# Kernel optimization log

Hardware: AMD Instinct MI355X
Metric: run time of the kernel (lower is better)

The kernel has to match this reference:

```python
import jax, jax.numpy as jnp
import numpy as np

NEG_SLOPE = 0.2


def setup_inputs() -> dict:
    key = jax.random.key(0)
    ks = jax.random.split(key, 10)
    V, E, Din, Dout, H = 50000, 800000, 128, 128, 4
    h = jax.random.normal(ks[0], (V, Din), dtype=jnp.float32)
    edge_index = jax.random.randint(ks[1], (2, E), 0, V, dtype=jnp.int32)
    edge_weight = jax.random.uniform(ks[2], (E,), dtype=jnp.float32)
    s = 1.0 / np.sqrt(Din)
    Wq = jax.random.normal(ks[3], (Din, Dout), dtype=jnp.float32) * s
    Wk = jax.random.normal(ks[4], (Din, Dout), dtype=jnp.float32) * s
    Wv = jax.random.normal(ks[5], (Din, Dout), dtype=jnp.float32) * s
    Wo = jax.random.normal(ks[6], (Dout, Dout), dtype=jnp.float32) * (1.0 / np.sqrt(Dout))
    We = jax.random.normal(ks[7], (1, H), dtype=jnp.float32)
    bq = jnp.zeros((Dout,), jnp.float32)
    bk = jnp.zeros((Dout,), jnp.float32)
    bv = jnp.zeros((Dout,), jnp.float32)
    bo = jnp.zeros((Dout,), jnp.float32)
    be = jnp.zeros((H,), jnp.float32)
    return {"h": h, "edge_index": edge_index, "edge_weight": edge_weight,
            "Wq": Wq, "bq": bq, "Wk": Wk, "bk": bk, "Wv": Wv, "bv": bv,
            "Wo": Wo, "bo": bo, "We": We, "be": be}


def reference(h, edge_index, edge_weight, Wq, bq, Wk, bk, Wv, bv, Wo, bo, We, be):
    V = h.shape[0]
    H = be.shape[0]
    Dout = Wq.shape[1]
    F_h = Dout // H

    # Node projections -> [V, H, F_h]
    Q = (h @ Wq + bq).reshape(V, H, F_h)
    K = (h @ Wk + bk).reshape(V, H, F_h)
    Vv = (h @ Wv + bv).reshape(V, H, F_h)

    # Edge bias: Linear(1, H) on edge_weight, then LeakyReLU -> [E, H]
    edge_bias = jax.nn.leaky_relu(edge_weight[:, None] @ We + be, negative_slope=NEG_SLOPE)

    src, tgt = edge_index[0], edge_index[1]

    # Per-edge attention logits: dot(Q[src], K[tgt]) / sqrt(F_h) + bias -> [E, H]
    attn_raw = jnp.sum(Q[src] * K[tgt], axis=-1) / jnp.sqrt(jnp.float32(F_h)) + edge_bias
    attn_exp = jnp.exp(attn_raw)  # faithful: original uses unshifted exp

    # Scatter-softmax normalizer per target node -> [V, H]
    deg = jax.ops.segment_sum(attn_exp, tgt, num_segments=V) + 1e-16
    attn_norm = attn_exp / deg[tgt]  # [E, H]

    # Weighted messages and scatter-sum to targets
    msg = Vv[src] * attn_norm[:, :, None] * edge_weight[:, None, None]  # [E, H, F_h]
    out = jax.ops.segment_sum(msg, tgt, num_segments=V)  # [V, H, F_h]

    out = out.reshape(V, H * F_h)
    out = jax.nn.leaky_relu(out @ Wo + bo, negative_slope=NEG_SLOPE)
    return out
```

## Files before the change

kernel.cpp:

```cpp
#include <hip/hip_runtime.h>
#include <hip/hip_bf16.h>

#define NEG_SLOPE 0.2f

typedef __attribute__((ext_vector_type(8))) short bf16x8;
typedef __attribute__((ext_vector_type(4))) float f32x4;

__device__ __forceinline__ void splitf(float x, unsigned short& h, unsigned short& l)
{
    const unsigned int u  = __float_as_uint(x);
    const unsigned int uh = (u + 0x7fffu + ((u >> 16) & 1u)) >> 16;
    const float        fh = __uint_as_float(uh << 16);
    const float        r  = x - fh;
    const unsigned int ur = __float_as_uint(r);
    const unsigned int ul = (ur + 0x7fffu + ((ur >> 16) & 1u)) >> 16;
    h = (unsigned short)uh;
    l = (unsigned short)ul;
}

__global__ __launch_bounds__(256) void wsplit(const float* __restrict__ W,
                                              unsigned short* __restrict__ Wth,
                                              unsigned short* __restrict__ Wtl)
{
    const int t = blockIdx.x * 256 + threadIdx.x;
    const int k = t >> 7, n = t & 127;
    unsigned short h, l;
    splitf(W[k * 128 + n], h, l);
    Wth[n * 128 + k] = h;
    Wtl[n * 128 + k] = l;
}

__global__ __launch_bounds__(256) void gemm_mfma(
    const float* __restrict__ A,
    const unsigned short* __restrict__ Bh0, const unsigned short* __restrict__ Bl0,
    const unsigned short* __restrict__ Bh1, const unsigned short* __restrict__ Bl1,
    const unsigned short* __restrict__ Bh2, const unsigned short* __restrict__ Bl2,
    const float* __restrict__ b0, const float* __restrict__ b1, const float* __restrict__ b2,
    float* __restrict__ D0, float* __restrict__ D1, float* __restrict__ D2,
    int V, int lrelu)
{
    __shared__ unsigned short Ash[64][40], Asl[64][40];
    __shared__ unsigned short Bsh[128][40], Bsl[128][40];

    const int m = blockIdx.y;
    const unsigned short* __restrict__ Wth = (m == 0) ? Bh0 : ((m == 1) ? Bh1 : Bh2);
    const unsigned short* __restrict__ Wtl = (m == 0) ? Bl0 : ((m == 1) ? Bl1 : Bl2);
    const float* __restrict__ bias         = (m == 0) ? b0  : ((m == 1) ? b1  : b2);
    float* __restrict__ D                  = (m == 0) ? D0  : ((m == 1) ? D1  : D2);

    const int tid  = threadIdx.x;
    const int w    = tid >> 6;
    const int l    = tid & 63;
    const int row0 = blockIdx.x * 64;

    const int srow = tid >> 2;
    const int skc  = tid & 3;

    f32x4 acc[8];
#pragma unroll
    for (int t = 0; t < 8; ++t) acc[t] = (f32x4){0.f, 0.f, 0.f, 0.f};

    for (int k0 = 0; k0 < 128; k0 += 32) {
        {
            const int gr = row0 + srow;
            float x[8] = {0.f, 0.f, 0.f, 0.f, 0.f, 0.f, 0.f, 0.f};
            if (gr < V) {
                const float4 a0 = *(const float4*)(A + (size_t)gr * 128 + k0 + skc * 8);
                const float4 a1 = *(const float4*)(A + (size_t)gr * 128 + k0 + skc * 8 + 4);
                x[0] = a0.x; x[1] = a0.y; x[2] = a0.z; x[3] = a0.w;
                x[4] = a1.x; x[5] = a1.y; x[6] = a1.z; x[7] = a1.w;
            }
            bf16x8 vh, vl;
#pragma unroll
            for (int i = 0; i < 8; ++i) {
                unsigned short hh, ll;
                splitf(x[i], hh, ll);
                vh[i] = (short)hh; vl[i] = (short)ll;
            }
            *(bf16x8*)&Ash[srow][skc * 8] = vh;
            *(bf16x8*)&Asl[srow][skc * 8] = vl;
        }
#pragma unroll
        for (int r = 0; r < 2; ++r) {
            const int idx = tid + r * 256;
            const int n = idx >> 2, bkc = idx & 3;
            *(bf16x8*)&Bsh[n][bkc * 8] = *(const bf16x8*)(Wth + n * 128 + k0 + bkc * 8);
            *(bf16x8*)&Bsl[n][bkc * 8] = *(const bf16x8*)(Wtl + n * 128 + k0 + bkc * 8);
        }
        __syncthreads();

        const int ar  = w * 16 + (l & 15);
        const int kc8 = (l >> 4) * 8;
        const bf16x8 ah = *(const bf16x8*)&Ash[ar][kc8];
        const bf16x8 al = *(const bf16x8*)&Asl[ar][kc8];
#pragma unroll
        for (int t = 0; t < 8; ++t) {
            const int col = t * 16 + (l & 15);
            const bf16x8 bh = *(const bf16x8*)&Bsh[col][kc8];
            const bf16x8 bl = *(const bf16x8*)&Bsl[col][kc8];
            acc[t] = __builtin_amdgcn_mfma_f32_16x16x32_bf16(ah, bh, acc[t], 0, 0, 0);
            acc[t] = __builtin_amdgcn_mfma_f32_16x16x32_bf16(ah, bl, acc[t], 0, 0, 0);
            acc[t] = __builtin_amdgcn_mfma_f32_16x16x32_bf16(al, bh, acc[t], 0, 0, 0);
        }
        __syncthreads();
    }

    const int colb = l & 15;
    const int rsub = (l >> 4) * 4;
#pragma unroll
    for (int t = 0; t < 8; ++t) {
        const int col = t * 16 + colb;
        const float bv = bias[col];
#pragma unroll
        for (int r = 0; r < 4; ++r) {
            const int grow = row0 + w * 16 + rsub + r;
            if (grow < V) {
                float xx = acc[t][r] + bv;
                if (lrelu) xx = (xx > 0.f) ? xx : NEG_SLOPE * xx;
                D[(size_t)grow * 128 + col] = xx;
            }
        }
    }
}

__global__ __launch_bounds__(256) void count_tgt(const int* __restrict__ tgt,
                                                 int* __restrict__ cnt, int E)
{
    const int e = blockIdx.x * blockDim.x + threadIdx.x;
    if (e < E) atomicAdd(cnt + tgt[e], 1);
}

__global__ __launch_bounds__(256) void scan1(const int* __restrict__ cnt,
                                             int* __restrict__ offs,
                                             int* __restrict__ bsums, int V)
{
    __shared__ int sh[256];
    const int t = threadIdx.x;
    const int base = blockIdx.x * 1024;
    int v[4];
    int s = 0;
#pragma unroll
    for (int i = 0; i < 4; ++i) {
        const int idx = base + t * 4 + i;
        v[i] = (idx < V) ? cnt[idx] : 0;
        s += v[i];
    }
    sh[t] = s;
    __syncthreads();
    for (int off = 1; off < 256; off <<= 1) {
        const int x = (t >= off) ? sh[t - off] : 0;
        __syncthreads();
        sh[t] += x;
        __syncthreads();
    }
    int run = (t > 0) ? sh[t - 1] : 0;
#pragma unroll
    for (int i = 0; i < 4; ++i) {
        const int idx = base + t * 4 + i;
        if (idx < V) offs[idx] = run;
        run += v[i];
    }
    if (t == 255) bsums[blockIdx.x] = sh[255];
}

__global__ void scan2(int* __restrict__ bsums, int nb)
{
    if (threadIdx.x == 0 && blockIdx.x == 0) {
        int run = 0;
        for (int i = 0; i < nb; ++i) { const int x = bsums[i]; bsums[i] = run; run += x; }
    }
}

__global__ __launch_bounds__(256) void scan3(int* __restrict__ offs,
                                             const int* __restrict__ bsums,
                                             int* __restrict__ fill, int V)
{
    const int v = blockIdx.x * blockDim.x + threadIdx.x;
    if (v >= V) return;
    const int o = offs[v] + bsums[v >> 10];
    offs[v] = o;
    fill[v] = o;
}

__global__ __launch_bounds__(256) void scatter_edges(
    const int* __restrict__ src, const int* __restrict__ tgt,
    const float* __restrict__ ew, int* __restrict__ fill,
    int2* __restrict__ se, int E)
{
    const int e = blockIdx.x * blockDim.x + threadIdx.x;
    if (e >= E) return;
    const int pos = atomicAdd(fill + tgt[e], 1);
    se[pos] = make_int2(src[e], __float_as_int(ew[e]));
}

__global__ __launch_bounds__(256) void fused_agg(
    const float* __restrict__ Q, const float* __restrict__ K,
    const float* __restrict__ Vv, const int2* __restrict__ se,
    const int* __restrict__ offs, const int* __restrict__ fill,
    const float* __restrict__ Wei, const float* __restrict__ bei,
    float* __restrict__ accum, int V)
{
    __shared__ float Ksh[4][4][36];
    const int wid = threadIdx.x >> 6;
    const int node = blockIdx.x * 4 + wid;
    if (node >= V) return;
    const int l   = threadIdx.x & 63;
    const int h   = l & 3;
    const int hd  = l >> 4;
    const float weH = Wei[h], beH = bei[h];
    const float2* __restrict__ Vv2 = (const float2*)Vv;

    {
        const float2 kk = *(const float2*)(K + (size_t)node * 128 + l * 2);
        const int f0 = l * 2;
        Ksh[wid][f0 >> 5][f0 & 31] = kk.x;
        Ksh[wid][(f0 + 1) >> 5][(f0 + 1) & 31] = kk.y;
    }

    const int start = offs[node];
    const int end   = fill[node];

    float degacc = 0.f;
    float ax = 0.f, ay = 0.f;

    for (int b0 = start; b0 < end; b0 += 16) {
        const int nj = min(16, end - b0);
        const int jj = l >> 2;
        int   s = 0;
        float w = 0.f, p = 0.f;
        if (jj < nj) {
            const int2 t = se[b0 + jj];
            s = t.x;
            w = __int_as_float(t.y);
            const float4* qp = (const float4*)(Q + (size_t)s * 128 + h * 32);
            float dot = 0.f;
#pragma unroll
            for (int i = 0; i < 8; ++i) {
                const float4 q = qp[i];
                const float4 k = *(const float4*)&Ksh[wid][h][i * 4];
                dot += q.x * k.x + q.y * k.y + q.z * k.z + q.w * k.w;
            }
            float bb = fmaf(w, weH, beH);
            bb = (bb > 0.f) ? bb : NEG_SLOPE * bb;
            p = __expf(fmaf(dot, 0.17677669529663687f, bb));
        }
        degacc += p;
        const float coef = p * w;

        if (nj == 16) {
#pragma unroll
            for (int j = 0; j < 16; ++j) {
                const float cj = __shfl(coef, j * 4 + hd);
                const int   sj = __shfl(s,    j * 4);
                const float2 v = Vv2[(size_t)sj * 64 + l];
                ax = fmaf(cj, v.x, ax);
                ay = fmaf(cj, v.y, ay);
            }
        } else {
            for (int j = 0; j < nj; ++j) {
                const float cj = __shfl(coef, j * 4 + hd);
                const int   sj = __shfl(s,    j * 4);
                const float2 v = Vv2[(size_t)sj * 64 + l];
                ax = fmaf(cj, v.x, ax);
                ay = fmaf(cj, v.y, ay);
            }
        }
    }

    float d = degacc;
    d += __shfl_xor(d, 4);
    d += __shfl_xor(d, 8);
    d += __shfl_xor(d, 16);
    d += __shfl_xor(d, 32);
    const float deg = __shfl(d, hd);
    const float inv = 1.0f / (deg + 1e-16f);

    *(float2*)(accum + (size_t)node * 128 + l * 2) =
        make_float2(ax * inv, ay * inv);
}

extern "C" void kernel_launch(void* const* d_in, const int* in_sizes, int n_in,
                              void* d_out, int out_size, void* d_ws, size_t ws_size,
                              hipStream_t stream)
{
    const float* h   = (const float*)d_in[0];
    const int*   ei  = (const int*)  d_in[1];
    const float* ew  = (const float*)d_in[2];
    const float* Wq  = (const float*)d_in[3];
    const float* bq  = (const float*)d_in[4];
    const float* Wk  = (const float*)d_in[5];
    const float* bk  = (const float*)d_in[6];
    const float* Wv  = (const float*)d_in[7];
    const float* bv  = (const float*)d_in[8];
    const float* Wo  = (const float*)d_in[9];
    const float* bo  = (const float*)d_in[10];
    const float* Wei = (const float*)d_in[11];
    const float* bei = (const float*)d_in[12];

    const int V = in_sizes[0] / 128;
    const int E = in_sizes[2];
    const int* src = ei;
    const int* tgt = ei + E;

    float* Q     = (float*)d_ws;
    float* Km    = Q  + (size_t)V * 128;
    float* Vm    = Km + (size_t)V * 128;
    float* accum = Vm + (size_t)V * 128;
    unsigned short* Wsp = (unsigned short*)(accum + (size_t)V * 128);
    unsigned short* WthQ = Wsp;
    unsigned short* WtlQ = Wsp + 16384;
    unsigned short* WthK = Wsp + 2 * 16384;
    unsigned short* WtlK = Wsp + 3 * 16384;
    unsigned short* WthV = Wsp + 4 * 16384;
    unsigned short* WtlV = Wsp + 5 * 16384;
    unsigned short* WthO = Wsp + 6 * 16384;
    unsigned short* WtlO = Wsp + 7 * 16384;
    int2*  se    = (int2*)(Wsp + 8 * 16384);
    int*   cnt   = (int*)(se + E);
    int*   offs  = cnt  + V;
    int*   fill  = offs + V + 1;
    int*   bsums = fill + V;

    hipMemsetAsync(cnt, 0, (size_t)V * sizeof(int), stream);

    wsplit<<<64, 256, 0, stream>>>(Wq, WthQ, WtlQ);
    wsplit<<<64, 256, 0, stream>>>(Wk, WthK, WtlK);
    wsplit<<<64, 256, 0, stream>>>(Wv, WthV, WtlV);
    wsplit<<<64, 256, 0, stream>>>(Wo, WthO, WtlO);

    const int mfGrid = (V + 63) / 64;
    gemm_mfma<<<dim3(mfGrid, 3), 256, 0, stream>>>(
        h, WthQ, WtlQ, WthK, WtlK, WthV, WtlV,
        bq, bk, bv, Q, Km, Vm, V, 0);

    count_tgt<<<(E + 255) / 256, 256, 0, stream>>>(tgt, cnt, E);
    const int nb = (V + 1023) / 1024;
    scan1<<<nb, 256, 0, stream>>>(cnt, offs, bsums, V);
    scan2<<<1, 64, 0, stream>>>(bsums, nb);
    scan3<<<(V + 255) / 256, 256, 0, stream>>>(offs, bsums, fill, V);
    scatter_edges<<<(E + 255) / 256, 256, 0, stream>>>(
        src, tgt, ew, fill, se, E);

    fused_agg<<<(V + 3) / 4, 256, 0, stream>>>(
        Q, Km, Vm, se, offs, fill, Wei, bei, accum, V);

    gemm_mfma<<<dim3(mfGrid, 1), 256, 0, stream>>>(
        accum, WthO, WtlO, WthO, WtlO, WthO, WtlO,
        bo, bo, bo, (float*)d_out, (float*)d_out, (float*)d_out, V, 1);
}
```

Before: 294.7 us.

## Merge prep kernels, single-block scan, and reuse A tile across QKV GEMMs

```diff
diff --git a/kernel.cpp b/kernel.cpp
--- a/kernel.cpp
+++ b/kernel.cpp
@@ -18,35 +18,169 @@
     l = (unsigned short)ul;
 }
 
-__global__ __launch_bounds__(256) void wsplit(const float* __restrict__ W,
-                                              unsigned short* __restrict__ Wth,
-                                              unsigned short* __restrict__ Wtl)
-{
-    const int t = blockIdx.x * 256 + threadIdx.x;
-    const int k = t >> 7, n = t & 127;
-    unsigned short h, l;
-    splitf(W[k * 128 + n], h, l);
-    Wth[n * 128 + k] = h;
-    Wtl[n * 128 + k] = l;
+__global__ __launch_bounds__(256) void prep(
+    const float* __restrict__ Wq, const float* __restrict__ Wk,
+    const float* __restrict__ Wv, const float* __restrict__ Wo,
+    unsigned short* __restrict__ Wth, unsigned short* __restrict__ Wtl,
+    const int* __restrict__ tgt, int* __restrict__ cnt, int E)
+{
+    const int bid = blockIdx.x;
+    if (bid < 256) {
+        const int mat = bid >> 6;
+        const float* __restrict__ W =
+            (mat == 0) ? Wq : ((mat == 1) ? Wk : ((mat == 2) ? Wv : Wo));
+        const int t = (bid & 63) * 256 + threadIdx.x;
+        const int k = t >> 7, n = t & 127;
+        unsigned short h, l;
+        splitf(W[k * 128 + n], h, l);
+        Wth[mat * 16384 + n * 128 + k] = h;
+        Wtl[mat * 16384 + n * 128 + k] = l;
+    } else {
+        const int e = (bid - 256) * 256 + threadIdx.x;
+        if (e < E) atomicAdd(cnt + tgt[e], 1);
+    }
+}
+
+__global__ __launch_bounds__(1024) void scan_all(
+    const int* __restrict__ cnt, int* __restrict__ offs,
+    int* __restrict__ fill, int V)
+{
+    __shared__ int sh[1024];
+    const int t = threadIdx.x;
+    const int per = (V + 1023) / 1024;
+    const int beg = min(t * per, V);
+    const int end = min(beg + per, V);
+    int s = 0;
+    for (int i = beg; i < end; ++i) s += cnt[i];
+    sh[t] = s;
+    __syncthreads();
+    for (int off = 1; off < 1024; off <<= 1) {
+        const int x = (t >= off) ? sh[t - off] : 0;
+        __syncthreads();
+        sh[t] += x;
+        __syncthreads();
+    }
+    int run = (t > 0) ? sh[t - 1] : 0;
+    for (int i = beg; i < end; ++i) {
+        offs[i] = run;
+        fill[i] = run;
+        run += cnt[i];
+    }
+}
+
+__global__ __launch_bounds__(256) void scatter_edges(
+    const int* __restrict__ src, const int* __restrict__ tgt,
+    const float* __restrict__ ew, int* __restrict__ fill,
+    int2* __restrict__ se, int E)
+{
+    const int e = blockIdx.x * blockDim.x + threadIdx.x;
+    if (e >= E) return;
+    const int pos = atomicAdd(fill + tgt[e], 1);
+    se[pos] = make_int2(src[e], __float_as_int(ew[e]));
+}
+
+__global__ __launch_bounds__(256) void gemm_qkv3(
+    const float* __restrict__ A,
+    const unsigned short* __restrict__ Wth, const unsigned short* __restrict__ Wtl,
+    const float* __restrict__ bq, const float* __restrict__ bk,
+    const float* __restrict__ bv,
+    float* __restrict__ D0, float* __restrict__ D1, float* __restrict__ D2,
+    int V)
+{
+    __shared__ unsigned short Ash[64][136], Asl[64][136];
+    __shared__ unsigned short Bsh[128][40], Bsl[128][40];
+
+    const int tid  = threadIdx.x;
+    const int w    = tid >> 6;
+    const int l    = tid & 63;
+    const int row0 = blockIdx.x * 64;
+
+    {
+        const int srow = tid >> 2;
+        const int sk0  = (tid & 3) * 32;
+        const int gr   = row0 + srow;
+#pragma unroll
+        for (int c = 0; c < 4; ++c) {
+            float x[8] = {0.f, 0.f, 0.f, 0.f, 0.f, 0.f, 0.f, 0.f};
+            if (gr < V) {
+                const float4 a0 = *(const float4*)(A + (size_t)gr * 128 + sk0 + c * 8);
+                const float4 a1 = *(const float4*)(A + (size_t)gr * 128 + sk0 + c * 8 + 4);
+                x[0] = a0.x; x[1] = a0.y; x[2] = a0.z; x[3] = a0.w;
+                x[4] = a1.x; x[5] = a1.y; x[6] = a1.z; x[7] = a1.w;
+            }
+            bf16x8 vh, vl;
+#pragma unroll
+            for (int i = 0; i < 8; ++i) {
+                unsigned short hh, ll;
+                splitf(x[i], hh, ll);
+                vh[i] = (short)hh; vl[i] = (short)ll;
+            }
+            *(bf16x8*)&Ash[srow][sk0 + c * 8] = vh;
+            *(bf16x8*)&Asl[srow][sk0 + c * 8] = vl;
+        }
+    }
+    __syncthreads();
+
+    const int ar   = w * 16 + (l & 15);
+    const int kc8  = (l >> 4) * 8;
+    const int colb = l & 15;
+    const int rsub = (l >> 4) * 4;
+
+    for (int m = 0; m < 3; ++m) {
+        const unsigned short* __restrict__ Wh = Wth + m * 16384;
+        const unsigned short* __restrict__ Wl = Wtl + m * 16384;
+        const float* __restrict__ bias = (m == 0) ? bq : ((m == 1) ? bk : bv);
+        float* __restrict__ D          = (m == 0) ? D0 : ((m == 1) ? D1 : D2);
+
+        f32x4 acc[8];
+#pragma unroll
+        for (int t = 0; t < 8; ++t) acc[t] = (f32x4){0.f, 0.f, 0.f, 0.f};
+
+        for (int k0 = 0; k0 < 128; k0 += 32) {
+#pragma unroll
+            for (int r = 0; r < 2; ++r) {
+                const int idx = tid + r * 256;
+                const int n = idx >> 2, bkc = (idx & 3) * 8;
+                *(bf16x8*)&Bsh[n][bkc] = *(const bf16x8*)(Wh + n * 128 + k0 + bkc);
+                *(bf16x8*)&Bsl[n][bkc] = *(const bf16x8*)(Wl + n * 128 + k0 + bkc);
+            }
+            __syncthreads();
+
+            const bf16x8 ah = *(const bf16x8*)&Ash[ar][k0 + kc8];
+            const bf16x8 al = *(const bf16x8*)&Asl[ar][k0 + kc8];
+#pragma unroll
+            for (int t = 0; t < 8; ++t) {
+                const int col = t * 16 + colb;
+                const bf16x8 bh = *(const bf16x8*)&Bsh[col][kc8];
+                const bf16x8 bl = *(const bf16x8*)&Bsl[col][kc8];
+                acc[t] = __builtin_amdgcn_mfma_f32_16x16x32_bf16(ah, bh, acc[t], 0, 0, 0);
+                acc[t] = __builtin_amdgcn_mfma_f32_16x16x32_bf16(ah, bl, acc[t], 0, 0, 0);
+                acc[t] = __builtin_amdgcn_mfma_f32_16x16x32_bf16(al, bh, acc[t], 0, 0, 0);
+            }
+            __syncthreads();
+        }
+
+#pragma unroll
+        for (int t = 0; t < 8; ++t) {
+            const int col = t * 16 + colb;
+            const float bv_ = bias[col];
+#pragma unroll
+            for (int r = 0; r < 4; ++r) {
+                const int grow = row0 + w * 16 + rsub + r;
+                if (grow < V)
+                    D[(size_t)grow * 128 + col] = acc[t][r] + bv_;
+            }
+        }
+    }
 }
 
 __global__ __launch_bounds__(256) void gemm_mfma(
     const float* __restrict__ A,
-    const unsigned short* __restrict__ Bh0, const unsigned short* __restrict__ Bl0,
-    const unsigned short* __restrict__ Bh1, const unsigned short* __restrict__ Bl1,
-    const unsigned short* __restrict__ Bh2, const unsigned short* __restrict__ Bl2,
-    const float* __restrict__ b0, const float* __restrict__ b1, const float* __restrict__ b2,
-    float* __restrict__ D0, float* __restrict__ D1, float* __restrict__ D2,
-    int V, int lrelu)
+    const unsigned short* __restrict__ Wth, const unsigned short* __restrict__ Wtl,
+    const float* __restrict__ bias, float* __restrict__ D, int V)
 {
     __shared__ unsigned short Ash[64][40], Asl[64][40];
     __shared__ unsigned short Bsh[128][40], Bsl[128][40];
-
-    const int m = blockIdx.y;
-    const unsigned short* __restrict__ Wth = (m == 0) ? Bh0 : ((m == 1) ? Bh1 : Bh2);
-    const unsigned short* __restrict__ Wtl = (m == 0) ? Bl0 : ((m == 1) ? Bl1 : Bl2);
-    const float* __restrict__ bias         = (m == 0) ? b0  : ((m == 1) ? b1  : b2);
-    float* __restrict__ D                  = (m == 0) ? D0  : ((m == 1) ? D1  : D2);
 
     const int tid  = threadIdx.x;
     const int w    = tid >> 6;
@@ -110,87 +244,17 @@
 #pragma unroll
     for (int t = 0; t < 8; ++t) {
         const int col = t * 16 + colb;
-        const float bv = bias[col];
+        const float bv_ = bias[col];
 #pragma unroll
         for (int r = 0; r < 4; ++r) {
             const int grow = row0 + w * 16 + rsub + r;
             if (grow < V) {
-                float xx = acc[t][r] + bv;
-                if (lrelu) xx = (xx > 0.f) ? xx : NEG_SLOPE * xx;
+                float xx = acc[t][r] + bv_;
+                xx = (xx > 0.f) ? xx : NEG_SLOPE * xx;
                 D[(size_t)grow * 128 + col] = xx;
             }
         }
     }
-}
-
-__global__ __launch_bounds__(256) void count_tgt(const int* __restrict__ tgt,
-                                                 int* __restrict__ cnt, int E)
-{
-    const int e = blockIdx.x * blockDim.x + threadIdx.x;
-    if (e < E) atomicAdd(cnt + tgt[e], 1);
-}
-
-__global__ __launch_bounds__(256) void scan1(const int* __restrict__ cnt,
-                                             int* __restrict__ offs,
-                                             int* __restrict__ bsums, int V)
-{
-    __shared__ int sh[256];
-    const int t = threadIdx.x;
-    const int base = blockIdx.x * 1024;
-    int v[4];
-    int s = 0;
-#pragma unroll
-    for (int i = 0; i < 4; ++i) {
-        const int idx = base + t * 4 + i;
-        v[i] = (idx < V) ? cnt[idx] : 0;
-        s += v[i];
-    }
-    sh[t] = s;
-    __syncthreads();
-    for (int off = 1; off < 256; off <<= 1) {
-        const int x = (t >= off) ? sh[t - off] : 0;
-        __syncthreads();
-        sh[t] += x;
-        __syncthreads();
-    }
-    int run = (t > 0) ? sh[t - 1] : 0;
-#pragma unroll
-    for (int i = 0; i < 4; ++i) {
-        const int idx = base + t * 4 + i;
-        if (idx < V) offs[idx] = run;
-        run += v[i];
-    }
-    if (t == 255) bsums[blockIdx.x] = sh[255];
-}
-
-__global__ void scan2(int* __restrict__ bsums, int nb)
-{
-    if (threadIdx.x == 0 && blockIdx.x == 0) {
-        int run = 0;
-        for (int i = 0; i < nb; ++i) { const int x = bsums[i]; bsums[i] = run; run += x; }
-    }
-}
-
-__global__ __launch_bounds__(256) void scan3(int* __restrict__ offs,
-                                             const int* __restrict__ bsums,
-                                             int* __restrict__ fill, int V)
-{
-    const int v = blockIdx.x * blockDim.x + threadIdx.x;
-    if (v >= V) return;
-    const int o = offs[v] + bsums[v >> 10];
-    offs[v] = o;
-    fill[v] = o;
-}
-
-__global__ __launch_bounds__(256) void scatter_edges(
-    const int* __restrict__ src, const int* __restrict__ tgt,
-    const float* __restrict__ ew, int* __restrict__ fill,
-    int2* __restrict__ se, int E)
-{
-    const int e = blockIdx.x * blockDim.x + threadIdx.x;
-    if (e >= E) return;
-    const int pos = atomicAdd(fill + tgt[e], 1);
-    se[pos] = make_int2(src[e], __float_as_int(ew[e]));
 }
 
 __global__ __launch_bounds__(256) void fused_agg(
@@ -306,45 +370,30 @@
     float* Km    = Q  + (size_t)V * 128;
     float* Vm    = Km + (size_t)V * 128;
     float* accum = Vm + (size_t)V * 128;
-    unsigned short* Wsp = (unsigned short*)(accum + (size_t)V * 128);
-    unsigned short* WthQ = Wsp;
-    unsigned short* WtlQ = Wsp + 16384;
-    unsigned short* WthK = Wsp + 2 * 16384;
-    unsigned short* WtlK = Wsp + 3 * 16384;
-    unsigned short* WthV = Wsp + 4 * 16384;
-    unsigned short* WtlV = Wsp + 5 * 16384;
-    unsigned short* WthO = Wsp + 6 * 16384;
-    unsigned short* WtlO = Wsp + 7 * 16384;
-    int2*  se    = (int2*)(Wsp + 8 * 16384);
+    unsigned short* Wth = (unsigned short*)(accum + (size_t)V * 128);
+    unsigned short* Wtl = Wth + 4 * 16384;
+    int2*  se    = (int2*)(Wtl + 4 * 16384);
     int*   cnt   = (int*)(se + E);
     int*   offs  = cnt  + V;
     int*   fill  = offs + V + 1;
-    int*   bsums = fill + V;
 
     hipMemsetAsync(cnt, 0, (size_t)V * sizeof(int), stream);
 
-    wsplit<<<64, 256, 0, stream>>>(Wq, WthQ, WtlQ);
-    wsplit<<<64, 256, 0, stream>>>(Wk, WthK, WtlK);
-    wsplit<<<64, 256, 0, stream>>>(Wv, WthV, WtlV);
-    wsplit<<<64, 256, 0, stream>>>(Wo, WthO, WtlO);
-
-    const int mfGrid = (V + 63) / 64;
-    gemm_mfma<<<dim3(mfGrid, 3), 256, 0, stream>>>(
-        h, WthQ, WtlQ, WthK, WtlK, WthV, WtlV,
-        bq, bk, bv, Q, Km, Vm, V, 0);
-
-    count_tgt<<<(E + 255) / 256, 256, 0, stream>>>(tgt, cnt, E);
-    const int nb = (V + 1023) / 1024;
-    scan1<<<nb, 256, 0, stream>>>(cnt, offs, bsums, V);
-    scan2<<<1, 64, 0, stream>>>(bsums, nb);
-    scan3<<<(V + 255) / 256, 256, 0, stream>>>(offs, bsums, fill, V);
+    prep<<<256 + (E + 255) / 256, 256, 0, stream>>>(
+        Wq, Wk, Wv, Wo, Wth, Wtl, tgt, cnt, E);
+
+    scan_all<<<1, 1024, 0, stream>>>(cnt, offs, fill, V);
+
     scatter_edges<<<(E + 255) / 256, 256, 0, stream>>>(
         src, tgt, ew, fill, se, E);
 
+    const int mfGrid = (V + 63) / 64;
+    gemm_qkv3<<<mfGrid, 256, 0, stream>>>(
+        h, Wth, Wtl, bq, bk, bv, Q, Km, Vm, V);
+
     fused_agg<<<(V + 3) / 4, 256, 0, stream>>>(
         Q, Km, Vm, se, offs, fill, Wei, bei, accum, V);
 
-    gemm_mfma<<<dim3(mfGrid, 1), 256, 0, stream>>>(
-        accum, WthO, WtlO, WthO, WtlO, WthO, WtlO,
-        bo, bo, bo, (float*)d_out, (float*)d_out, (float*)d_out, V, 1);
-}
+    gemm_mfma<<<mfGrid, 256, 0, stream>>>(
+        accum, Wth + 3 * 16384, Wtl + 3 * 16384, bo, (float*)d_out, V);
+}
```

New measurement: 394.4 us. 1.34x slower.
